# Optimization experiments

Measured on AMD Instinct MI355X. Metric: run time of the kernel, lower is better.

The kernel has to match this reference:

```python
import jax, jax.numpy as jnp
import numpy as np

EPS = 1e-5
TEMP = 0.1

def conv3x3(x, w, b):
    y = jax.lax.conv_general_dilated(x, w, window_strides=(1, 1), padding=((1, 1), (1, 1)),
                                     dimension_numbers=('NCHW', 'OIHW', 'NCHW'))
    return y + b[None, :, None, None]

def batchnorm_train(x, gamma, beta):
    # torch BatchNorm2d training-mode normalization (biased variance)
    mean = jnp.mean(x, axis=(0, 2, 3), keepdims=True)
    var = jnp.var(x, axis=(0, 2, 3), keepdims=True)
    xn = (x - mean) * jax.lax.rsqrt(var + EPS)
    return xn * gamma[None, :, None, None] + beta[None, :, None, None]

def basis_pool(x, pw, pb):
    # x: [B,C,H,W]; pw,pb: [K] (1x1 conv from 1 channel to K basis channels)
    # kernel=stride=2 => non-overlapping 2x2 patches
    B, C, H, W = x.shape
    K = pw.shape[0]
    oh, ow = H // 2, W // 2
    # patches [B,C,oh,ow,4] in (dh,dw) row-major order (matches F.unfold)
    patches = x.reshape(B, C, oh, 2, ow, 2).transpose(0, 1, 2, 4, 3, 5).reshape(B, C, oh, ow, 4)
    # per-channel 1x1 projection -> scores [B,C,K,H,W]
    scores = x[:, :, None] * pw[None, None, :, None, None] + pb[None, None, :, None, None]
    sp = scores.reshape(B, C, K, oh, 2, ow, 2).transpose(0, 1, 2, 3, 5, 4, 6).reshape(B, C, K, oh, ow, 4)
    wts = jax.nn.softmax(sp / TEMP, axis=-1)
    # softmax-weighted sum over the 4 patch elements -> [B,C,K,oh,ow]
    bv = jnp.einsum('bchwp,bckhwp->bckhw', patches, wts)
    # interleave channels as c*K + k (matches torch output layout)
    return bv.reshape(B, C * K, oh, ow)

def setup_inputs() -> dict:
    key = jax.random.key(0)
    ks = jax.random.split(key, 16)
    d = {}
    d['x'] = jax.random.normal(ks[0], (1024, 3, 32, 32), dtype=jnp.float32)
    d['conv1_w'] = jax.random.normal(ks[1], (16, 3, 3, 3), dtype=jnp.float32) * 0.1
    d['conv1_b'] = jax.random.normal(ks[2], (16,), dtype=jnp.float32) * 0.01
    d['bn1_g'] = jnp.ones((16,), jnp.float32)
    d['bn1_b'] = jnp.zeros((16,), jnp.float32)
    d['proj1_w'] = jax.random.normal(ks[3], (2,), dtype=jnp.float32)
    d['proj1_b'] = jax.random.normal(ks[4], (2,), dtype=jnp.float32) * 0.01
    d['conv2_w'] = jax.random.normal(ks[5], (32, 32, 3, 3), dtype=jnp.float32) * 0.06
    d['conv2_b'] = jax.random.normal(ks[6], (32,), dtype=jnp.float32) * 0.01
    d['bn2_g'] = jnp.ones((32,), jnp.float32)
    d['bn2_b'] = jnp.zeros((32,), jnp.float32)
    d['proj2_w'] = jax.random.normal(ks[7], (2,), dtype=jnp.float32)
    d['proj2_b'] = jax.random.normal(ks[8], (2,), dtype=jnp.float32) * 0.01
    d['fc_w'] = jax.random.normal(ks[9], (10, 32 * 2 * 8 * 8), dtype=jnp.float32) * 0.02
    d['fc_b'] = jnp.zeros((10,), jnp.float32)
    return d

def reference(x, conv1_w, conv1_b, bn1_g, bn1_b, proj1_w, proj1_b,
              conv2_w, conv2_b, bn2_g, bn2_b, proj2_w, proj2_b, fc_w, fc_b):
    h = jax.nn.relu(batchnorm_train(conv3x3(x, conv1_w, conv1_b), bn1_g, bn1_b))
    h = basis_pool(h, proj1_w, proj1_b)  # [B,32,16,16]
    h = jax.nn.relu(batchnorm_train(conv3x3(h, conv2_w, conv2_b), bn2_g, bn2_b))
    h = basis_pool(h, proj2_w, proj2_b)  # [B,64,8,8]
    h = h.reshape(h.shape[0], -1)
    return h @ fc_w.T + fc_b
```

## Files before the change

kernel.cpp:

```cpp
#include <hip/hip_runtime.h>

#define EPSV 1e-5f

typedef __attribute__((ext_vector_type(8))) short bf16x8;
typedef __attribute__((ext_vector_type(4))) float f32x4;

__device__ __forceinline__ unsigned short f2bf(float x) {
  unsigned u = __float_as_uint(x);
  unsigned r = (u + 0x7FFFu + ((u >> 16) & 1u)) >> 16;
  return (unsigned short)r;
}

__device__ __forceinline__ float block_reduce_sum(float v, float* lds) {
  #pragma unroll
  for (int off = 32; off > 0; off >>= 1) v += __shfl_down(v, off, 64);
  int lane = threadIdx.x & 63;
  int wid  = threadIdx.x >> 6;
  __syncthreads();
  if (lane == 0) lds[wid] = v;
  __syncthreads();
  float r = 0.f;
  if (threadIdx.x == 0) {
    int nw = blockDim.x >> 6;
    for (int i = 0; i < nw; ++i) r += lds[i];
  }
  return r;
}

__device__ __forceinline__ void stage_x(const float* __restrict__ x, float* xt, int b, int tid) {
  {
    float4* t4 = (float4*)xt;
    #pragma unroll
    for (int i = 0; i < 4; ++i) {
      int idx = i * 256 + tid;
      if (idx < 867) t4[idx] = make_float4(0.f, 0.f, 0.f, 0.f);
    }
  }
  __syncthreads();
  {
    const float4* x4 = (const float4*)(x + b * 3072);
    #pragma unroll
    for (int k = 0; k < 3; ++k) {
      int e4 = k * 256 + tid;
      float4 v = x4[e4];
      int w0 = e4 * 4;
      int ch = w0 >> 10;
      int pos = w0 & 1023;
      int r = pos >> 5, c = pos & 31;
      int base = ch * 1156 + (r + 1) * 34 + (c + 1);
      xt[base] = v.x; xt[base + 1] = v.y; xt[base + 2] = v.z; xt[base + 3] = v.w;
    }
  }
  __syncthreads();
}

__global__ __launch_bounds__(256) void k1_conv1_stats(
    const float* __restrict__ x, const float* __restrict__ w1, const float* __restrict__ b1,
    float* __restrict__ partials ,
    const float* __restrict__ w2, short* __restrict__ wA) {
  __shared__ float xt[3468];
  __shared__ float red[64];
  const int tid = threadIdx.x, b = blockIdx.x;
  const int co0 = blockIdx.y * 8;

  if (b == 0) {
    for (int i = tid + blockIdx.y * 9216; i < (blockIdx.y + 1) * 9216; i += 256) {
      int e = i & 7, l = (i >> 3) & 63, p = (i >> 9) & 1, m = (i >> 10) & 1, s = i >> 11;
      int co = m * 16 + (l & 15);
      int ci = (l >> 4) * 8 + e;
      int ky = s / 3, kx = s - ky * 3;
      float wv = w2[((co * 32 + ci) * 3 + ky) * 3 + kx];
      unsigned short h = f2bf(wv);
      unsigned short val = p ? f2bf(wv - __uint_as_float((unsigned)h << 16)) : h;
      wA[i] = (short)val;
    }
  }

  stage_x(x, xt, b, tid);

  const int c = tid & 31, r0 = (tid >> 5) * 4;
  const int sbase = r0 * 34 + c;
  float xv[54];
  #pragma unroll
  for (int ci = 0; ci < 3; ++ci)
    #pragma unroll
    for (int dr = 0; dr < 6; ++dr)
      #pragma unroll
      for (int dx = 0; dx < 3; ++dx)
        xv[ci * 18 + dr * 3 + dx] = xt[ci * 1156 + sbase + dr * 34 + dx];

  const int lane = tid & 63, wid = tid >> 6;
  #pragma unroll
  for (int cl = 0; cl < 8; ++cl) {
    const int co = co0 + cl;
    float a0, a1, a2, a3;
    a0 = a1 = a2 = a3 = b1[co];
    #pragma unroll
    for (int ci = 0; ci < 3; ++ci)
      #pragma unroll
      for (int ky = 0; ky < 3; ++ky)
        #pragma unroll
        for (int kx = 0; kx < 3; ++kx) {
          float w = w1[co * 27 + ci * 9 + ky * 3 + kx];
          a0 = fmaf(xv[ci * 18 + (0 + ky) * 3 + kx], w, a0);
          a1 = fmaf(xv[ci * 18 + (1 + ky) * 3 + kx], w, a1);
          a2 = fmaf(xv[ci * 18 + (2 + ky) * 3 + kx], w, a2);
          a3 = fmaf(xv[ci * 18 + (3 + ky) * 3 + kx], w, a3);
        }
    float s = a0 + a1 + a2 + a3;
    float q = fmaf(a0, a0, fmaf(a1, a1, fmaf(a2, a2, a3 * a3)));
    #pragma unroll
    for (int o = 32; o > 0; o >>= 1) {
      s += __shfl_down(s, o, 64);
      q += __shfl_down(q, o, 64);
    }
    if (lane == 0) { red[wid * 16 + cl * 2] = s; red[wid * 16 + cl * 2 + 1] = q; }
  }
  __syncthreads();
  if (tid < 16) {
    int cl = tid >> 1, sel = tid & 1;
    float r = red[cl * 2 + sel] + red[16 + cl * 2 + sel] +
              red[32 + cl * 2 + sel] + red[48 + cl * 2 + sel];
    partials[((co0 + cl) * 2 + sel) * 1024 + b] = r;
  }
}

__global__ __launch_bounds__(256) void k_bn_finalize(
    const float* __restrict__ partials, int nb, float invN,
    const float* __restrict__ gamma, const float* __restrict__ beta,
    float* __restrict__ stats, int C) {
  __shared__ float lds[4];
  int c = blockIdx.x;
  float s = 0.f, q = 0.f;
  for (int i = threadIdx.x; i < nb; i += blockDim.x) {
    s += partials[(c * 2 + 0) * nb + i];
    q += partials[(c * 2 + 1) * nb + i];
  }
  s = block_reduce_sum(s, lds);
  q = block_reduce_sum(q, lds);
  if (threadIdx.x == 0) {
    float mean = s * invN;
    float var  = q * invN - mean * mean;
    float scale = gamma[c] * rsqrtf(var + EPSV);
    stats[c]     = scale;
    stats[C + c] = beta[c] - mean * scale;
  }
}

__global__ __launch_bounds__(256) void k34_pool1_conv2(
    const float* __restrict__ x, const float* __restrict__ w1, const float* __restrict__ b1,
    const float* __restrict__ stats1, const float* __restrict__ pw, const float* __restrict__ pb,
    const short* __restrict__ wA, const float* __restrict__ b2,
    float* __restrict__ y2, float* __restrict__ partials) {
  __shared__ __align__(16) short bh[25920];
  const int tid = threadIdx.x, b = blockIdx.x;

  float* xt = (float*)bh;
  stage_x(x, xt, b, tid);

  const int ow = tid & 15, oh = tid >> 4;
  const int wbase = (2 * oh) * 34 + 2 * ow;
  float xv[48];
  #pragma unroll
  for (int ci = 0; ci < 3; ++ci)
    #pragma unroll
    for (int dr = 0; dr < 4; ++dr)
      #pragma unroll
      for (int dx = 0; dx < 4; ++dx)
        xv[ci * 16 + dr * 4 + dx] = xt[ci * 1156 + wbase + dr * 34 + dx];
  __syncthreads();

  for (int t = tid; t < 680; t += 256) {
    int plane = t >= 340;
    int u = plane ? t - 340 : t;
    int i = u / 5, part = u - i * 5;
    int r, cc;
    if (i < 18)      { r = 0;  cc = i; }
    else if (i < 36) { r = 17; cc = i - 18; }
    else { int j = i - 36; r = 1 + (j >> 1); cc = (j & 1) * 17; }
    *(int4*)&bh[plane * 12960 + (r * 18 + cc) * 40 + part * 8] = make_int4(0, 0, 0, 0);
  }

  {
    const float pw0 = pw[0] * 10.f, pw1 = pw[1] * 10.f;
    const float pb0 = pb[0] * 10.f, pb1 = pb[1] * 10.f;
    unsigned hiw[16], low[16];
    #pragma unroll
    for (int c = 0; c < 16; ++c) {
      const float scale = stats1[c], shift = stats1[16 + c];
      float v[4];
      #pragma unroll
      for (int p = 0; p < 4; ++p) {
        int dh = p >> 1, dw = p & 1;
        float a = b1[c];
        #pragma unroll
        for (int ci = 0; ci < 3; ++ci)
          #pragma unroll
          for (int ky = 0; ky < 3; ++ky)
            #pragma unroll
            for (int kx = 0; kx < 3; ++kx)
              a = fmaf(xv[ci * 16 + (dh + ky) * 4 + (dw + kx)], w1[(c * 3 + ci) * 9 + ky * 3 + kx], a);
        a = fmaf(a, scale, shift);
        v[p] = fmaxf(a, 0.f);
      }
      float o0, o1;
      #pragma unroll
      for (int k = 0; k < 2; ++k) {
        float cw = k ? pw1 : pw0;
        float cb = k ? pb1 : pb0;
        float s0 = fmaf(v[0], cw, cb), s1 = fmaf(v[1], cw, cb);
        float s2 = fmaf(v[2], cw, cb), s3 = fmaf(v[3], cw, cb);
        float m = fmaxf(fmaxf(s0, s1), fmaxf(s2, s3));
        float e0 = expf(s0 - m), e1 = expf(s1 - m), e2 = expf(s2 - m), e3 = expf(s3 - m);
        float den = e0 + e1 + e2 + e3;
        float outv = (v[0] * e0 + v[1] * e1 + v[2] * e2 + v[3] * e3) / den;
        if (k == 0) o0 = outv; else o1 = outv;
      }
      unsigned short h0 = f2bf(o0), h1 = f2bf(o1);
      float f0 = __uint_as_float((unsigned)h0 << 16);
      float f1 = __uint_as_float((unsigned)h1 << 16);
      unsigned short l0 = f2bf(o0 - f0), l1 = f2bf(o1 - f1);
      hiw[c] = (unsigned)h0 | ((unsigned)h1 << 16);
      low[c] = (unsigned)l0 | ((unsigned)l1 << 16);
    }
    const int cell = (oh + 1) * 18 + (ow + 1);
    #pragma unroll
    for (int k = 0; k < 4; ++k) *(int4*)&bh[cell * 40 + k * 8]         = *(int4*)&hiw[k * 4];
    #pragma unroll
    for (int k = 0; k < 4; ++k) *(int4*)&bh[12960 + cell * 40 + k * 8] = *(int4*)&low[k * 4];
  }
  __syncthreads();

  const int l = tid & 63;
  const int w = tid >> 6;
  const int q = l >> 4;
  const int c = l & 15;
  const int rbase = w * 4;

  f32x4 acc[2][4];
  #pragma unroll
  for (int m = 0; m < 2; ++m) {
    f32x4 bj = *(const f32x4*)&b2[m * 16 + q * 4];
    #pragma unroll
    for (int r = 0; r < 4; ++r) acc[m][r] = bj;
  }

  const bf16x8* wAf = (const bf16x8*)wA;
  for (int ky = 0; ky < 3; ++ky) {
    for (int kx = 0; kx < 3; ++kx) {
      const int s = ky * 3 + kx;
      bf16x8 a0h = wAf[((s * 2 + 0) * 2 + 0) * 64 + l];
      bf16x8 a0l = wAf[((s * 2 + 0) * 2 + 1) * 64 + l];
      bf16x8 a1h = wAf[((s * 2 + 1) * 2 + 0) * 64 + l];
      bf16x8 a1l = wAf[((s * 2 + 1) * 2 + 1) * 64 + l];
      #pragma unroll
      for (int r = 0; r < 4; ++r) {
        const int pos = (rbase + r + ky) * 18 + (c + kx);
        bf16x8 bhv = *(const bf16x8*)&bh[pos * 40 + q * 8];
        bf16x8 blv = *(const bf16x8*)&bh[12960 + pos * 40 + q * 8];
        acc[0][r] = __builtin_amdgcn_mfma_f32_16x16x32_bf16(a0h, bhv, acc[0][r], 0, 0, 0);
        acc[0][r] = __builtin_amdgcn_mfma_f32_16x16x32_bf16(a0h, blv, acc[0][r], 0, 0, 0);
        acc[0][r] = __builtin_amdgcn_mfma_f32_16x16x32_bf16(a0l, bhv, acc[0][r], 0, 0, 0);
        acc[1][r] = __builtin_amdgcn_mfma_f32_16x16x32_bf16(a1h, bhv, acc[1][r], 0, 0, 0);
        acc[1][r] = __builtin_amdgcn_mfma_f32_16x16x32_bf16(a1h, blv, acc[1][r], 0, 0, 0);
        acc[1][r] = __builtin_amdgcn_mfma_f32_16x16x32_bf16(a1l, bhv, acc[1][r], 0, 0, 0);
      }
    }
  }

  {
    float* yb = y2 + b * 8192;
    #pragma unroll
    for (int m = 0; m < 2; ++m)
      #pragma unroll
      for (int r = 0; r < 4; ++r)
        #pragma unroll
        for (int j = 0; j < 4; ++j)
          yb[(m * 16 + q * 4 + j) * 256 + (rbase + r) * 16 + c] = acc[m][r][j];
  }

  const int slot = b * 4 + w;
  #pragma unroll
  for (int m = 0; m < 2; ++m) {
    #pragma unroll
    for (int j = 0; j < 4; ++j) {
      float a0 = acc[m][0][j], a1 = acc[m][1][j], a2 = acc[m][2][j], a3 = acc[m][3][j];
      float sv = a0 + a1 + a2 + a3;
      float qv = fmaf(a0, a0, fmaf(a1, a1, fmaf(a2, a2, a3 * a3)));
      #pragma unroll
      for (int o = 1; o <= 8; o <<= 1) {
        sv += __shfl_xor(sv, o, 64);
        qv += __shfl_xor(qv, o, 64);
      }
      if (c == 0) {
        int co = m * 16 + q * 4 + j;
        partials[(co * 2 + 0) * 4096 + slot] = sv;
        partials[(co * 2 + 1) * 4096 + slot] = qv;
      }
    }
  }
}

__global__ __launch_bounds__(256) void k78_pool2_fc(
    const float* __restrict__ y2, const float* __restrict__ stats2,
    const float* __restrict__ pw, const float* __restrict__ pb,
    const float* __restrict__ fcw, const float* __restrict__ fcb,
    float* __restrict__ out) {
  __shared__ float h2s[4096];
  __shared__ float red[40];
  const int tid = threadIdx.x;
  const int b = blockIdx.x;

  {
    const int c = tid >> 3, oh = tid & 7;
    const float scale = stats2[c], shift = stats2[32 + c];
    const float pw0 = pw[0] * 10.f, pw1 = pw[1] * 10.f;
    const float pb0 = pb[0] * 10.f, pb1 = pb[1] * 10.f;
    const float* yb = y2 + (b * 32 + c) * 256 + (2 * oh) * 16;
    float rowa[16], rowb[16];
    #pragma unroll
    for (int k = 0; k < 4; ++k) {
      *(float4*)&rowa[k * 4] = ((const float4*)yb)[k];
      *(float4*)&rowb[k * 4] = ((const float4*)(yb + 16))[k];
    }
    #pragma unroll
    for (int ow = 0; ow < 8; ++ow) {
      float v0 = fmaxf(fmaf(rowa[2 * ow],     scale, shift), 0.f);
      float v1 = fmaxf(fmaf(rowa[2 * ow + 1], scale, shift), 0.f);
      float v2 = fmaxf(fmaf(rowb[2 * ow],     scale, shift), 0.f);
      float v3 = fmaxf(fmaf(rowb[2 * ow + 1], scale, shift), 0.f);
      #pragma unroll
      for (int k = 0; k < 2; ++k) {
        float cw = k ? pw1 : pw0;
        float cb = k ? pb1 : pb0;
        float s0 = fmaf(v0, cw, cb), s1 = fmaf(v1, cw, cb);
        float s2 = fmaf(v2, cw, cb), s3 = fmaf(v3, cw, cb);
        float m = fmaxf(fmaxf(s0, s1), fmaxf(s2, s3));
        float e0 = expf(s0 - m), e1 = expf(s1 - m), e2 = expf(s2 - m), e3 = expf(s3 - m);
        float den = e0 + e1 + e2 + e3;
        h2s[(c * 2 + k) * 64 + oh * 8 + ow] =
            (v0 * e0 + v1 * e1 + v2 * e2 + v3 * e3) / den;
      }
    }
  }
  __syncthreads();

  float acc[10];
  #pragma unroll
  for (int j = 0; j < 10; ++j) acc[j] = 0.f;
  #pragma unroll
  for (int k = 0; k < 16; ++k) {
    float hv = h2s[k * 256 + tid];
    #pragma unroll
    for (int j = 0; j < 10; ++j)
      acc[j] = fmaf(hv, fcw[j * 4096 + k * 256 + tid], acc[j]);
  }
  const int lane = tid & 63, wid = tid >> 6;
  #pragma unroll
  for (int j = 0; j < 10; ++j) {
    float v = acc[j];
    #pragma unroll
    for (int off = 32; off > 0; off >>= 1) v += __shfl_down(v, off, 64);
    if (lane == 0) red[wid * 10 + j] = v;
  }
  __syncthreads();
  if (tid < 10) {
    out[b * 10 + tid] = red[tid] + red[10 + tid] + red[20 + tid] + red[30 + tid] + fcb[tid];
  }
}

extern "C" void kernel_launch(void* const* d_in, const int* in_sizes, int n_in,
                              void* d_out, int out_size, void* d_ws, size_t ws_size,
                              hipStream_t stream) {
  (void)in_sizes; (void)n_in; (void)out_size; (void)ws_size;
  const float* x   = (const float*)d_in[0];
  const float* w1  = (const float*)d_in[1];
  const float* b1  = (const float*)d_in[2];
  const float* g1  = (const float*)d_in[3];
  const float* be1 = (const float*)d_in[4];
  const float* pw1 = (const float*)d_in[5];
  const float* pb1 = (const float*)d_in[6];
  const float* w2  = (const float*)d_in[7];
  const float* b2  = (const float*)d_in[8];
  const float* g2  = (const float*)d_in[9];
  const float* be2 = (const float*)d_in[10];
  const float* pw2 = (const float*)d_in[11];
  const float* pb2 = (const float*)d_in[12];
  const float* fcw = (const float*)d_in[13];
  const float* fcb = (const float*)d_in[14];
  float* out = (float*)d_out;

  char* ws = (char*)d_ws;
  float* y2       = (float*)(ws);
  float* partials = (float*)(ws + 33554432);
  short* wA       = (short*)(ws + 33554432 + 1048576);
  float* stats1   = (float*)(ws + 33554432 + 1048576 + 36864);
  float* stats2   = stats1 + 32;

  dim3 g2d(1024, 2);
  k1_conv1_stats<<<g2d, 256, 0, stream>>>(x, w1, b1, partials, w2, wA);
  k_bn_finalize<<<16, 256, 0, stream>>>(partials, 1024, 1.f / 1048576.f, g1, be1, stats1, 16);
  k34_pool1_conv2<<<1024, 256, 0, stream>>>(x, w1, b1, stats1, pw1, pb1, wA, b2, y2, partials);
  k_bn_finalize<<<32, 256, 0, stream>>>(partials, 4096, 1.f / 262144.f, g2, be2, stats2, 32);
  k78_pool2_fc<<<1024, 256, 0, stream>>>(y2, stats2, pw2, pb2, fcw, fcb, out);
}
```

Measured before the change: 104.1 us.

## Double block size of fused pool1/conv2 kernel, splitting channels and rows across waves

The fused pool1+conv2 kernel now runs 512 threads per block instead of 256. Each thread computes 8 of the 16 conv1 channels for its pooled cell, and each of the 8 waves handles 2 output rows instead of 4. The input staging is inlined, the partial-stats buffer doubles to 8192 slots, and the workspace offsets move to fit it. The aim is more wave-level parallelism per block and lower register pressure per thread, so latency is hidden better. The cost is duplicated xv loads per thread and a larger partial-statistics reduction in the BN finalize step.

Measured after the change: 107.6 us. 1.03x slower.

```diff
diff --git a/kernel.cpp b/kernel.cpp
--- a/kernel.cpp
+++ b/kernel.cpp
@@ -147,7 +147,7 @@
   }
 }
 
-__global__ __launch_bounds__(256) void k34_pool1_conv2(
+__global__ __launch_bounds__(512, 4) void k34_pool1_conv2(
     const float* __restrict__ x, const float* __restrict__ w1, const float* __restrict__ b1,
     const float* __restrict__ stats1, const float* __restrict__ pw, const float* __restrict__ pb,
     const short* __restrict__ wA, const float* __restrict__ b2,
@@ -156,9 +156,28 @@
   const int tid = threadIdx.x, b = blockIdx.x;
 
   float* xt = (float*)bh;
-  stage_x(x, xt, b, tid);
-
-  const int ow = tid & 15, oh = tid >> 4;
+  {
+    float4* t4 = (float4*)xt;
+    for (int idx = tid; idx < 867; idx += 512) t4[idx] = make_float4(0.f, 0.f, 0.f, 0.f);
+  }
+  __syncthreads();
+  {
+    const float4* x4 = (const float4*)(x + b * 3072);
+    for (int e4 = tid; e4 < 768; e4 += 512) {
+      float4 v = x4[e4];
+      int w0 = e4 * 4;
+      int ch = w0 >> 10;
+      int pos = w0 & 1023;
+      int r = pos >> 5, c = pos & 31;
+      int base = ch * 1156 + (r + 1) * 34 + (c + 1);
+      xt[base] = v.x; xt[base + 1] = v.y; xt[base + 2] = v.z; xt[base + 3] = v.w;
+    }
+  }
+  __syncthreads();
+
+  const int cell = tid & 255;
+  const int chalf = tid >> 8;
+  const int ow = cell & 15, oh = cell >> 4;
   const int wbase = (2 * oh) * 34 + 2 * ow;
   float xv[48];
   #pragma unroll
@@ -170,7 +189,7 @@
         xv[ci * 16 + dr * 4 + dx] = xt[ci * 1156 + wbase + dr * 34 + dx];
   __syncthreads();
 
-  for (int t = tid; t < 680; t += 256) {
+  for (int t = tid; t < 680; t += 512) {
     int plane = t >= 340;
     int u = plane ? t - 340 : t;
     int i = u / 5, part = u - i * 5;
@@ -184,9 +203,10 @@
   {
     const float pw0 = pw[0] * 10.f, pw1 = pw[1] * 10.f;
     const float pb0 = pb[0] * 10.f, pb1 = pb[1] * 10.f;
-    unsigned hiw[16], low[16];
-    #pragma unroll
-    for (int c = 0; c < 16; ++c) {
+    unsigned hiw[8], low[8];
+    #pragma unroll
+    for (int cl = 0; cl < 8; ++cl) {
+      const int c = chalf * 8 + cl;
       const float scale = stats1[c], shift = stats1[16 + c];
       float v[4];
       #pragma unroll
@@ -220,14 +240,16 @@
       float f0 = __uint_as_float((unsigned)h0 << 16);
       float f1 = __uint_as_float((unsigned)h1 << 16);
       unsigned short l0 = f2bf(o0 - f0), l1 = f2bf(o1 - f1);
-      hiw[c] = (unsigned)h0 | ((unsigned)h1 << 16);
-      low[c] = (unsigned)l0 | ((unsigned)l1 << 16);
-    }
-    const int cell = (oh + 1) * 18 + (ow + 1);
-    #pragma unroll
-    for (int k = 0; k < 4; ++k) *(int4*)&bh[cell * 40 + k * 8]         = *(int4*)&hiw[k * 4];
-    #pragma unroll
-    for (int k = 0; k < 4; ++k) *(int4*)&bh[12960 + cell * 40 + k * 8] = *(int4*)&low[k * 4];
+      hiw[cl] = (unsigned)h0 | ((unsigned)h1 << 16);
+      low[cl] = (unsigned)l0 | ((unsigned)l1 << 16);
+    }
+    const int pcell = (oh + 1) * 18 + (ow + 1);
+    short* hp = &bh[pcell * 40 + chalf * 16];
+    *(int4*)hp       = *(int4*)&hiw[0];
+    *(int4*)(hp + 8) = *(int4*)&hiw[4];
+    short* lp = &bh[12960 + pcell * 40 + chalf * 16];
+    *(int4*)lp       = *(int4*)&low[0];
+    *(int4*)(lp + 8) = *(int4*)&low[4];
   }
   __syncthreads();
 
@@ -235,14 +257,13 @@
   const int w = tid >> 6;
   const int q = l >> 4;
   const int c = l & 15;
-  const int rbase = w * 4;
-
-  f32x4 acc[2][4];
+  const int rbase = w * 2;
+
+  f32x4 acc[2][2];
   #pragma unroll
   for (int m = 0; m < 2; ++m) {
     f32x4 bj = *(const f32x4*)&b2[m * 16 + q * 4];
-    #pragma unroll
-    for (int r = 0; r < 4; ++r) acc[m][r] = bj;
+    acc[m][0] = bj; acc[m][1] = bj;
   }
 
   const bf16x8* wAf = (const bf16x8*)wA;
@@ -254,7 +275,7 @@
       bf16x8 a1h = wAf[((s * 2 + 1) * 2 + 0) * 64 + l];
       bf16x8 a1l = wAf[((s * 2 + 1) * 2 + 1) * 64 + l];
       #pragma unroll
-      for (int r = 0; r < 4; ++r) {
+      for (int r = 0; r < 2; ++r) {
         const int pos = (rbase + r + ky) * 18 + (c + kx);
         bf16x8 bhv = *(const bf16x8*)&bh[pos * 40 + q * 8];
         bf16x8 blv = *(const bf16x8*)&bh[12960 + pos * 40 + q * 8];
@@ -273,20 +294,20 @@
     #pragma unroll
     for (int m = 0; m < 2; ++m)
       #pragma unroll
-      for (int r = 0; r < 4; ++r)
+      for (int r = 0; r < 2; ++r)
         #pragma unroll
         for (int j = 0; j < 4; ++j)
           yb[(m * 16 + q * 4 + j) * 256 + (rbase + r) * 16 + c] = acc[m][r][j];
   }
 
-  const int slot = b * 4 + w;
+  const int slot = b * 8 + w;
   #pragma unroll
   for (int m = 0; m < 2; ++m) {
     #pragma unroll
     for (int j = 0; j < 4; ++j) {
-      float a0 = acc[m][0][j], a1 = acc[m][1][j], a2 = acc[m][2][j], a3 = acc[m][3][j];
-      float sv = a0 + a1 + a2 + a3;
-      float qv = fmaf(a0, a0, fmaf(a1, a1, fmaf(a2, a2, a3 * a3)));
+      float a0 = acc[m][0][j], a1 = acc[m][1][j];
+      float sv = a0 + a1;
+      float qv = fmaf(a0, a0, a1 * a1);
       #pragma unroll
       for (int o = 1; o <= 8; o <<= 1) {
         sv += __shfl_xor(sv, o, 64);
@@ -294,8 +315,8 @@
       }
       if (c == 0) {
         int co = m * 16 + q * 4 + j;
-        partials[(co * 2 + 0) * 4096 + slot] = sv;
-        partials[(co * 2 + 1) * 4096 + slot] = qv;
+        partials[(co * 2 + 0) * 8192 + slot] = sv;
+        partials[(co * 2 + 1) * 8192 + slot] = qv;
       }
     }
   }
@@ -393,14 +414,14 @@
   char* ws = (char*)d_ws;
   float* y2       = (float*)(ws);
   float* partials = (float*)(ws + 33554432);
-  short* wA       = (short*)(ws + 33554432 + 1048576);
-  float* stats1   = (float*)(ws + 33554432 + 1048576 + 36864);
+  short* wA       = (short*)(ws + 33554432 + 2097152);
+  float* stats1   = (float*)(ws + 33554432 + 2097152 + 36864);
   float* stats2   = stats1 + 32;
 
   dim3 g2d(1024, 2);
   k1_conv1_stats<<<g2d, 256, 0, stream>>>(x, w1, b1, partials, w2, wA);
   k_bn_finalize<<<16, 256, 0, stream>>>(partials, 1024, 1.f / 1048576.f, g1, be1, stats1, 16);
-  k34_pool1_conv2<<<1024, 256, 0, stream>>>(x, w1, b1, stats1, pw1, pb1, wA, b2, y2, partials);
-  k_bn_finalize<<<32, 256, 0, stream>>>(partials, 4096, 1.f / 262144.f, g2, be2, stats2, 32);
+  k34_pool1_conv2<<<1024, 512, 0, stream>>>(x, w1, b1, stats1, pw1, pb1, wA, b2, y2, partials);
+  k_bn_finalize<<<32, 256, 0, stream>>>(partials, 8192, 1.f / 262144.f, g2, be2, stats2, 32);
   k78_pool2_fc<<<1024, 256, 0, stream>>>(y2, stats2, pw2, pb2, fcw, fcb, out);
 }
```
